# Optimization experiments

Measured on AMD Instinct MI355X. Metric: run time of the kernel, lower is better.

The kernel has to match this reference:

```python
import jax, jax.numpy as jnp
import numpy as np

B, T, H, FUTURE = 2048, 2048, 51, 128


def setup_inputs() -> dict:
    key = jax.random.key(0)
    ks = jax.random.split(key, 7)
    s = 1.0 / np.sqrt(H)  # PyTorch LSTMCell/Linear init range
    u = lambda k, shape: jax.random.uniform(k, shape, jnp.float32, -s, s)
    return {
        "x": jax.random.normal(ks[0], (B, T), jnp.float32),
        "W_ih": u(ks[1], (4 * H, 1)),
        "W_hh": u(ks[2], (4 * H, H)),
        "b_ih": u(ks[3], (4 * H,)),
        "b_hh": u(ks[4], (4 * H,)),
        "fc_w": u(ks[5], (1, H)),
        "fc_b": u(ks[6], (1,)),
        "future": FUTURE,
    }


def _lstm_cell(h, c, inp, W_ih, W_hh, b):
    # inp: [B, 1], h/c: [B, H]; PyTorch gate order: i, f, g, o
    gates = inp @ W_ih.T + h @ W_hh.T + b  # [B, 4H]
    i, f, g, o = jnp.split(gates, 4, axis=1)
    c_new = jax.nn.sigmoid(f) * c + jax.nn.sigmoid(i) * jnp.tanh(g)
    h_new = jax.nn.sigmoid(o) * jnp.tanh(c_new)
    return h_new, c_new


def reference(x, W_ih, W_hh, b_ih, b_hh, fc_w, fc_b, future):
    Bn = x.shape[0]
    Hn = W_hh.shape[1]
    b = b_ih + b_hh
    h0 = jnp.zeros((Bn, Hn), x.dtype)
    c0 = jnp.zeros((Bn, Hn), x.dtype)
    xs = x.T[:, :, None]  # [T, B, 1]

    def step(carry, inp_t):
        h, c = carry
        h, c = _lstm_cell(h, c, inp_t, W_ih, W_hh, b)
        out = h @ fc_w.T + fc_b  # [B, 1]
        return (h, c), out

    (h, c), outs = jax.lax.scan(step, (h0, c0), xs)  # outs: [T, B, 1]

    if future > 0:
        def fstep(carry, _):
            h, c, out = carry
            h, c = _lstm_cell(h, c, out, W_ih, W_hh, b)
            out = h @ fc_w.T + fc_b
            return (h, c, out), out

        _, fouts = jax.lax.scan(fstep, (h, c, outs[-1]), None, length=future)
        outs = jnp.concatenate([outs, fouts], axis=0)

    return outs[:, :, 0].T  # [B, T + future]
```

## Files before the change

kernel.cpp:

```cpp
#include <hip/hip_runtime.h>


typedef _Float16 v2h __attribute__((ext_vector_type(2)));
typedef float    v4f __attribute__((ext_vector_type(4)));

constexpr int Hh = 51;

__device__ __forceinline__ float fexp2(float x){ return __builtin_amdgcn_exp2f(x); }
__device__ __forceinline__ float frcp(float x) { return __builtin_amdgcn_rcpf(x); }
__device__ __forceinline__ float sigm(float x) { return frcp(1.f + fexp2(-1.44269504f * x)); }
__device__ __forceinline__ float tanh_f(float x){ return 1.f - 2.f * frcp(1.f + fexp2(2.88539008f * x)); }

__device__ __forceinline__ float rdlane(float v, int lane){
  return __int_as_float(__builtin_amdgcn_readlane(__float_as_int(v), lane));
}

__device__ __forceinline__ v2h bch(float f){
  union { float f; v2h h; } u; u.f = f; return u.h;
}

#if __has_builtin(__builtin_amdgcn_fdot2)
__device__ __forceinline__ float dot2(v2h a, v2h b, float c){
  return __builtin_amdgcn_fdot2(a, b, c, false);
}
#else
__device__ __forceinline__ float dot2(v2h a, v2h b, float c){
  float r;
  asm("v_dot2_f32_f16 %0, %1, %2, %3" : "=v"(r) : "v"(a), "v"(b), "v"(c));
  return r;
}
#endif

__global__ __launch_bounds__(64)
__attribute__((amdgpu_waves_per_eu(1)))
void lstm_kernel(const float* __restrict__ x,
                 const float* __restrict__ W_ih,
                 const float* __restrict__ W_hh,
                 const float* __restrict__ b_ih,
                 const float* __restrict__ b_hh,
                 const float* __restrict__ fc_w,
                 const float* __restrict__ fc_b,
                 float* __restrict__ out,
                 int T, int OT)
{
  const int k   = threadIdx.x;
  const int row = blockIdx.x;

  __shared__ __align__(16) _Float16 hbuf16[64];
  __shared__ float st[64][65];

  hbuf16[k] = (_Float16)0.f;

  const int kc = (k < Hh) ? k : (Hh - 1);
  v2h w0[26], w1[26], w2[26], w3[26];
  const long r0 = (long)(0 * Hh + kc) * Hh;
  const long r1 = (long)(1 * Hh + kc) * Hh;
  const long r2 = (long)(2 * Hh + kc) * Hh;
  const long r3 = (long)(3 * Hh + kc) * Hh;
#pragma unroll
  for (int m = 0; m < 25; ++m) {
    w0[m] = (v2h){(_Float16)W_hh[r0 + 2*m], (_Float16)W_hh[r0 + 2*m + 1]};
    w1[m] = (v2h){(_Float16)W_hh[r1 + 2*m], (_Float16)W_hh[r1 + 2*m + 1]};
    w2[m] = (v2h){(_Float16)W_hh[r2 + 2*m], (_Float16)W_hh[r2 + 2*m + 1]};
    w3[m] = (v2h){(_Float16)W_hh[r3 + 2*m], (_Float16)W_hh[r3 + 2*m + 1]};
  }
  w0[25] = (v2h){(_Float16)W_hh[r0 + 50], (_Float16)0.f};
  w1[25] = (v2h){(_Float16)W_hh[r1 + 50], (_Float16)0.f};
  w2[25] = (v2h){(_Float16)W_hh[r2 + 50], (_Float16)0.f};
  w3[25] = (v2h){(_Float16)W_hh[r3 + 50], (_Float16)0.f};
  const float wi0 = W_ih[0 * Hh + kc], wi1 = W_ih[1 * Hh + kc];
  const float wi2 = W_ih[2 * Hh + kc], wi3 = W_ih[3 * Hh + kc];
  const float bs0 = b_ih[0 * Hh + kc] + b_hh[0 * Hh + kc];
  const float bs1 = b_ih[1 * Hh + kc] + b_hh[1 * Hh + kc];
  const float bs2 = b_ih[2 * Hh + kc] + b_hh[2 * Hh + kc];
  const float bs3 = b_ih[3 * Hh + kc] + b_hh[3 * Hh + kc];
  const float fcw = (k < Hh) ? fc_w[k] : 0.f;
  const float fcb = fc_b[0];

  float c = 0.f, h = 0.f;

  auto cell = [&](float xt) {
    float a0 = fmaf(xt, wi0, bs0);
    float a1 = fmaf(xt, wi1, bs1);
    float a2 = fmaf(xt, wi2, bs2);
    float a3 = fmaf(xt, wi3, bs3);
    const v4f* hb4 = (const v4f*)hbuf16;
#pragma unroll
    for (int q = 0; q < 7; ++q) {
      const v4f hv = hb4[q];
      const int p = 4 * q;
      const v2h h0 = bch(hv.x), h1 = bch(hv.y), h2 = bch(hv.z), h3 = bch(hv.w);
      a0 = dot2(w0[p], h0, a0);
      a1 = dot2(w1[p], h0, a1);
      a2 = dot2(w2[p], h0, a2);
      a3 = dot2(w3[p], h0, a3);
      if (p + 1 < 26) {
        a0 = dot2(w0[p+1], h1, a0); a1 = dot2(w1[p+1], h1, a1);
        a2 = dot2(w2[p+1], h1, a2); a3 = dot2(w3[p+1], h1, a3);
      }
      if (p + 2 < 26) {
        a0 = dot2(w0[p+2], h2, a0); a1 = dot2(w1[p+2], h2, a1);
        a2 = dot2(w2[p+2], h2, a2); a3 = dot2(w3[p+2], h2, a3);
      }
      if (p + 3 < 26) {
        a0 = dot2(w0[p+3], h3, a0); a1 = dot2(w1[p+3], h3, a1);
        a2 = dot2(w2[p+3], h3, a2); a3 = dot2(w3[p+3], h3, a3);
      }
    }
    const float ia = sigm(a0);
    const float fa = sigm(a1);
    const float ga = tanh_f(a2);
    const float oa = sigm(a3);
    c = fmaf(fa, c, ia * ga);
    h = oa * tanh_f(c);
    asm volatile("" ::: "memory");
    hbuf16[k] = (_Float16)h;
    asm volatile("" ::: "memory");
  };

  float s = fcb;
  for (int tc = 0; tc < T; tc += 64) {
    const float xv = x[(long)row * T + tc + k];
#pragma unroll 1
    for (int i = 0; i < 64; ++i) {
      cell(rdlane(xv, i));
      st[k][i] = h * fcw;
    }
    s = fcb;
#pragma unroll
    for (int j = 0; j < 64; ++j) s += st[j][k];
    asm volatile("" ::: "memory");
    out[(long)row * OT + tc + k] = s;
  }

  float out_prev = rdlane(s, 63);
  float obuf = 0.f;
  for (int t = T; t < OT; ++t) {
    cell(out_prev);
    float p = h * fcw;
#pragma unroll
    for (int off = 32; off > 0; off >>= 1) p += __shfl_xor(p, off, 64);
    const float out_t = p + fcb;
    obuf = (k == (t & 63)) ? out_t : obuf;
    if ((t & 63) == 63)
      out[(long)row * OT + (t - 63) + k] = obuf;
    out_prev = out_t;
  }
}

extern "C" void kernel_launch(void* const* d_in, const int* in_sizes, int n_in,
                              void* d_out, int out_size, void* d_ws, size_t ws_size,
                              hipStream_t stream) {
  const float* x    = (const float*)d_in[0];
  const float* W_ih = (const float*)d_in[1];
  const float* W_hh = (const float*)d_in[2];
  const float* b_ih = (const float*)d_in[3];
  const float* b_hh = (const float*)d_in[4];
  const float* fc_w = (const float*)d_in[5];
  const float* fc_b = (const float*)d_in[6];
  float* out = (float*)d_out;

  const int B  = 2048;
  const int T  = in_sizes[0] / B;
  const int OT = out_size / B;

  lstm_kernel<<<dim3(B), dim3(64), 0, stream>>>(x, W_ih, W_hh, b_ih, b_hh,
                                                fc_w, fc_b, out, T, OT);
}
```

Measured before the change: 1.299 ms.

## Fold input weight, log2e scaling and FC projection into the packed dot products

Weights and biases are prescaled by log2(e) so the gate activations skip a multiply. The input x is packed into the unused high half of the last h pair, so the input term rides in the existing dot2 chain instead of separate FMAs. An idle lane (52) is repurposed to compute the FC output from the previous h within the same dot loop, which removes the shared-memory transpose buffer and the 64-term column reduction. The cost is that x and the FC weights are now carried in fp16, which adds rounding error.

```diff
diff --git a/kernel.cpp b/kernel.cpp
--- a/kernel.cpp
+++ b/kernel.cpp
@@ -8,8 +8,9 @@
 
 __device__ __forceinline__ float fexp2(float x){ return __builtin_amdgcn_exp2f(x); }
 __device__ __forceinline__ float frcp(float x) { return __builtin_amdgcn_rcpf(x); }
-__device__ __forceinline__ float sigm(float x) { return frcp(1.f + fexp2(-1.44269504f * x)); }
-__device__ __forceinline__ float tanh_f(float x){ return 1.f - 2.f * frcp(1.f + fexp2(2.88539008f * x)); }
+__device__ __forceinline__ float sigm_p(float a){ return frcp(1.f + fexp2(-a)); }
+__device__ __forceinline__ float tanh_p(float a){ return 1.f - 2.f * frcp(1.f + fexp2(a + a)); }
+__device__ __forceinline__ float tanh_c(float x){ return 1.f - 2.f * frcp(1.f + fexp2(2.88539008f * x)); }
 
 __device__ __forceinline__ float rdlane(float v, int lane){
   return __int_as_float(__builtin_amdgcn_readlane(__float_as_int(v), lane));
@@ -18,18 +19,14 @@
 __device__ __forceinline__ v2h bch(float f){
   union { float f; v2h h; } u; u.f = f; return u.h;
 }
+__device__ __forceinline__ v2h ovr_hi(float f, unsigned hi16){
+  unsigned u = (__float_as_uint(f) & 0xFFFFu) | (hi16 << 16);
+  union { unsigned u; v2h h; } c; c.u = u; return c.h;
+}
 
-#if __has_builtin(__builtin_amdgcn_fdot2)
 __device__ __forceinline__ float dot2(v2h a, v2h b, float c){
   return __builtin_amdgcn_fdot2(a, b, c, false);
 }
-#else
-__device__ __forceinline__ float dot2(v2h a, v2h b, float c){
-  float r;
-  asm("v_dot2_f32_f16 %0, %1, %2, %3" : "=v"(r) : "v"(a), "v"(b), "v"(c));
-  return r;
-}
-#endif
 
 __global__ __launch_bounds__(64)
 __attribute__((amdgpu_waves_per_eu(1)))
@@ -45,9 +42,9 @@
 {
   const int k   = threadIdx.x;
   const int row = blockIdx.x;
+  const float S = 1.44269504089f;
 
   __shared__ __align__(16) _Float16 hbuf16[64];
-  __shared__ float st[64][65];
 
   hbuf16[k] = (_Float16)0.f;
 
@@ -59,37 +56,42 @@
   const long r3 = (long)(3 * Hh + kc) * Hh;
 #pragma unroll
   for (int m = 0; m < 25; ++m) {
-    w0[m] = (v2h){(_Float16)W_hh[r0 + 2*m], (_Float16)W_hh[r0 + 2*m + 1]};
-    w1[m] = (v2h){(_Float16)W_hh[r1 + 2*m], (_Float16)W_hh[r1 + 2*m + 1]};
-    w2[m] = (v2h){(_Float16)W_hh[r2 + 2*m], (_Float16)W_hh[r2 + 2*m + 1]};
-    w3[m] = (v2h){(_Float16)W_hh[r3 + 2*m], (_Float16)W_hh[r3 + 2*m + 1]};
+    w0[m] = (v2h){(_Float16)(S*W_hh[r0 + 2*m]), (_Float16)(S*W_hh[r0 + 2*m + 1])};
+    w1[m] = (v2h){(_Float16)(S*W_hh[r1 + 2*m]), (_Float16)(S*W_hh[r1 + 2*m + 1])};
+    w2[m] = (v2h){(_Float16)(S*W_hh[r2 + 2*m]), (_Float16)(S*W_hh[r2 + 2*m + 1])};
+    w3[m] = (v2h){(_Float16)(S*W_hh[r3 + 2*m]), (_Float16)(S*W_hh[r3 + 2*m + 1])};
   }
-  w0[25] = (v2h){(_Float16)W_hh[r0 + 50], (_Float16)0.f};
-  w1[25] = (v2h){(_Float16)W_hh[r1 + 50], (_Float16)0.f};
-  w2[25] = (v2h){(_Float16)W_hh[r2 + 50], (_Float16)0.f};
-  w3[25] = (v2h){(_Float16)W_hh[r3 + 50], (_Float16)0.f};
-  const float wi0 = W_ih[0 * Hh + kc], wi1 = W_ih[1 * Hh + kc];
-  const float wi2 = W_ih[2 * Hh + kc], wi3 = W_ih[3 * Hh + kc];
-  const float bs0 = b_ih[0 * Hh + kc] + b_hh[0 * Hh + kc];
-  const float bs1 = b_ih[1 * Hh + kc] + b_hh[1 * Hh + kc];
-  const float bs2 = b_ih[2 * Hh + kc] + b_hh[2 * Hh + kc];
-  const float bs3 = b_ih[3 * Hh + kc] + b_hh[3 * Hh + kc];
+  w0[25] = (v2h){(_Float16)(S*W_hh[r0 + 50]), (_Float16)(S*W_ih[0*Hh + kc])};
+  w1[25] = (v2h){(_Float16)(S*W_hh[r1 + 50]), (_Float16)(S*W_ih[1*Hh + kc])};
+  w2[25] = (v2h){(_Float16)(S*W_hh[r2 + 50]), (_Float16)(S*W_ih[2*Hh + kc])};
+  w3[25] = (v2h){(_Float16)(S*W_hh[r3 + 50]), (_Float16)(S*W_ih[3*Hh + kc])};
+  float bs0 = S*(b_ih[0*Hh + kc] + b_hh[0*Hh + kc]);
+  const float bs1 = S*(b_ih[1*Hh + kc] + b_hh[1*Hh + kc]);
+  const float bs2 = S*(b_ih[2*Hh + kc] + b_hh[2*Hh + kc]);
+  const float bs3 = S*(b_ih[3*Hh + kc] + b_hh[3*Hh + kc]);
   const float fcw = (k < Hh) ? fc_w[k] : 0.f;
   const float fcb = fc_b[0];
 
+  if (k == 52) {
+#pragma unroll
+    for (int m = 0; m < 25; ++m)
+      w0[m] = (v2h){(_Float16)fc_w[2*m], (_Float16)fc_w[2*m + 1]};
+    w0[25] = (v2h){(_Float16)fc_w[50], (_Float16)0.f};
+    bs0 = fcb;
+  }
+
   float c = 0.f, h = 0.f;
 
-  auto cell = [&](float xt) {
-    float a0 = fmaf(xt, wi0, bs0);
-    float a1 = fmaf(xt, wi1, bs1);
-    float a2 = fmaf(xt, wi2, bs2);
-    float a3 = fmaf(xt, wi3, bs3);
+  auto cell = [&](unsigned xu16) -> float {
+    float a0 = bs0, a1 = bs1, a2 = bs2, a3 = bs3;
     const v4f* hb4 = (const v4f*)hbuf16;
 #pragma unroll
     for (int q = 0; q < 7; ++q) {
       const v4f hv = hb4[q];
       const int p = 4 * q;
-      const v2h h0 = bch(hv.x), h1 = bch(hv.y), h2 = bch(hv.z), h3 = bch(hv.w);
+      const v2h h0 = bch(hv.x);
+      const v2h h1 = (q == 6) ? ovr_hi(hv.y, xu16) : bch(hv.y);
+      const v2h h2 = bch(hv.z), h3 = bch(hv.w);
       a0 = dot2(w0[p], h0, a0);
       a1 = dot2(w1[p], h0, a1);
       a2 = dot2(w2[p], h0, a2);
@@ -107,40 +109,53 @@
         a2 = dot2(w2[p+3], h3, a2); a3 = dot2(w3[p+3], h3, a3);
       }
     }
-    const float ia = sigm(a0);
-    const float fa = sigm(a1);
-    const float ga = tanh_f(a2);
-    const float oa = sigm(a3);
+    const float ia = sigm_p(a0);
+    const float fa = sigm_p(a1);
+    const float ga = tanh_p(a2);
+    const float oa = sigm_p(a3);
     c = fmaf(fa, c, ia * ga);
-    h = oa * tanh_f(c);
+    h = oa * tanh_c(c);
     asm volatile("" ::: "memory");
     hbuf16[k] = (_Float16)h;
     asm volatile("" ::: "memory");
+    return a0;
   };
 
-  float s = fcb;
+  float obuf = 0.f;
+
   for (int tc = 0; tc < T; tc += 64) {
     const float xv = x[(long)row * T + tc + k];
+    const unsigned xhu =
+        (unsigned)__builtin_bit_cast(unsigned short, (_Float16)xv);
 #pragma unroll 1
     for (int i = 0; i < 64; ++i) {
-      cell(rdlane(xv, i));
-      st[k][i] = h * fcw;
+      const int t = tc + i;
+      const unsigned xu = (unsigned)__builtin_amdgcn_readlane((int)xhu, i);
+      const float a0v = cell(xu);
+      const float o = rdlane(a0v, 52);
+      if (t > 0) {
+        obuf = (k == ((t - 1) & 63)) ? o : obuf;
+        if (((t - 1) & 63) == 63)
+          out[(long)row * OT + (t - 64) + k] = obuf;
+      }
     }
-    s = fcb;
-#pragma unroll
-    for (int j = 0; j < 64; ++j) s += st[j][k];
-    asm volatile("" ::: "memory");
-    out[(long)row * OT + tc + k] = s;
   }
 
-  float out_prev = rdlane(s, 63);
-  float obuf = 0.f;
+  float p = h * fcw;
+#pragma unroll
+  for (int off = 32; off > 0; off >>= 1) p += __shfl_xor(p, off, 64);
+  float out_prev = p + fcb;
+  obuf = (k == 63) ? out_prev : obuf;
+  out[(long)row * OT + (T - 64) + k] = obuf;
+
   for (int t = T; t < OT; ++t) {
-    cell(out_prev);
-    float p = h * fcw;
+    const unsigned xu =
+        (unsigned)__builtin_bit_cast(unsigned short, (_Float16)out_prev);
+    cell(xu);
+    float q = h * fcw;
 #pragma unroll
-    for (int off = 32; off > 0; off >>= 1) p += __shfl_xor(p, off, 64);
-    const float out_t = p + fcb;
+    for (int off = 32; off > 0; off >>= 1) q += __shfl_xor(q, off, 64);
+    const float out_t = q + fcb;
     obuf = (k == (t & 63)) ? out_t : obuf;
     if ((t & 63) == 63)
       out[(long)row * OT + (t - 63) + k] = obuf;
```

Result: no change. 1.323 ms (+1.8%).
